# Kernel tuning notes

Measured on AMD Instinct MI355X. Metric: run time of the kernel, lower is better.

Reference implementation:

```python
import jax, jax.numpy as jnp
import numpy as np

D = 256; NH = 8; HD = D // NH; L = 4; P = 4; NQ = 900; BS = 8; DFFN = 1024
SHAPES = np.array([[128, 128], [64, 64], [32, 32], [16, 16]])  # (H, W) per level, static metadata
NV = int((SHAPES[:, 0] * SHAPES[:, 1]).sum())
EPS = 1e-6


def setup_inputs():
    key = jax.random.key(0)
    ks = iter(jax.random.split(key, 48))

    def nrm(shape, scale=0.02):
        return jax.random.normal(next(ks), shape, jnp.float32) * scale

    lsi = np.concatenate([[0], np.cumsum(SHAPES[:, 0] * SHAPES[:, 1])[:-1]]).astype(np.int64)
    return {
        'tgt': nrm((NQ, BS, D), 1.0),
        'tgt_query_pos': nrm((NQ, BS, D), 1.0),
        'tgt_reference_points': jax.random.uniform(next(ks), (NQ, BS, L, 2), jnp.float32),
        'memory': nrm((NV, BS, D), 1.0),
        'memory_spatial_shapes': jnp.asarray(SHAPES, jnp.int32),
        'memory_level_start_index': jnp.asarray(lsi, jnp.int32),
        'w_norm_sa': jnp.ones((D,), jnp.float32),
        'w_norm_ca': jnp.ones((D,), jnp.float32),
        'w_norm_ffn': jnp.ones((D,), jnp.float32),
        'ls_sa': jnp.full((D,), 1e-4, jnp.float32),
        'ls_ca': jnp.full((D,), 1e-4, jnp.float32),
        'ls_ffn': jnp.full((D,), 1e-4, jnp.float32),
        'Wq': nrm((D, D)), 'Wk': nrm((D, D)), 'Wv': nrm((D, D)),
        'bq': jnp.zeros((D,), jnp.float32), 'bk': jnp.zeros((D,), jnp.float32), 'bv': jnp.zeros((D,), jnp.float32),
        'Wo_sa': nrm((D, D)), 'bo_sa': jnp.zeros((D,), jnp.float32),
        'Wv_proj': nrm((D, D)), 'bv_proj': jnp.zeros((D,), jnp.float32),
        'W_off': nrm((NH * L * P * 2, D)), 'b_off': nrm((NH * L * P * 2,), 0.1),
        'W_attn': nrm((NH * L * P, D)), 'b_attn': jnp.zeros((NH * L * P,), jnp.float32),
        'W_out_ca': nrm((D, D)), 'bo_ca': jnp.zeros((D,), jnp.float32),
        'Wg': nrm((DFFN, D)), 'bg': jnp.zeros((DFFN,), jnp.float32),
        'Wu': nrm((DFFN, D)), 'bu': jnp.zeros((DFFN,), jnp.float32),
        'Wf': nrm((D, DFFN)), 'bf': jnp.zeros((D,), jnp.float32),
    }


def rmsnorm(x, w):
    return x * jax.lax.rsqrt(jnp.mean(x * x, axis=-1, keepdims=True) + EPS) * w


def ms_deform_sample(v, loc, attw):
    # v: (bs, nv, NH, HD); loc: (bs, nq, NH, L, P, 2) normalized (x, y); attw: (bs, nq, NH, L, P)
    bs, nq = loc.shape[0], loc.shape[1]
    out = jnp.zeros((bs, nq, NH, HD), loc.dtype)
    b_idx = jnp.arange(bs)[:, None, None, None]
    h_idx = jnp.arange(NH)[None, None, :, None]
    start = 0
    for l in range(L):
        Hl, Wl = int(SHAPES[l, 0]), int(SHAPES[l, 1])
        vf = v[:, start:start + Hl * Wl]  # (bs, Hl*Wl, NH, HD)
        start += Hl * Wl
        # grid_sample(align_corners=False, padding=zeros) pixel mapping
        x = loc[:, :, :, l, :, 0] * Wl - 0.5
        y = loc[:, :, :, l, :, 1] * Hl - 0.5
        x0 = jnp.floor(x)
        y0 = jnp.floor(y)
        acc = jnp.zeros((bs, nq, NH, P, HD), loc.dtype)
        for dx in (0, 1):
            for dy in (0, 1):
                xi = x0 + dx
                yi = y0 + dy
                w = (1.0 - jnp.abs(x - xi)) * (1.0 - jnp.abs(y - yi))
                valid = (xi >= 0) & (xi <= Wl - 1) & (yi >= 0) & (yi <= Hl - 1)
                w = jnp.where(valid, w, 0.0)
                idx = (jnp.clip(yi, 0, Hl - 1) * Wl + jnp.clip(xi, 0, Wl - 1)).astype(jnp.int32)
                acc = acc + w[..., None] * vf[b_idx, idx, h_idx]  # (bs, nq, NH, P, HD)
        out = out + jnp.einsum('bqhp,bqhpd->bqhd', attw[:, :, :, l], acc)
    return out


def reference(tgt, tgt_query_pos, tgt_reference_points, memory, memory_spatial_shapes,
              memory_level_start_index, w_norm_sa, w_norm_ca, w_norm_ffn, ls_sa, ls_ca, ls_ffn,
              Wq, Wk, Wv, bq, bk, bv, Wo_sa, bo_sa, Wv_proj, bv_proj, W_off, b_off, W_attn,
              b_attn, W_out_ca, bo_ca, Wg, bg, Wu, bu, Wf, bf):
    nq, bs, d = tgt.shape
    # --- self-attention (pre-norm + LayerScale residual) ---
    xn = rmsnorm(tgt, w_norm_sa)
    qk = xn + tgt_query_pos
    q = (qk @ Wq.T + bq).reshape(nq, bs, NH, HD)
    k = (qk @ Wk.T + bk).reshape(nq, bs, NH, HD)
    vv = (xn @ Wv.T + bv).reshape(nq, bs, NH, HD)
    scores = jnp.einsum('qbhd,kbhd->bhqk', q, k) * (1.0 / np.sqrt(HD))
    attn = jax.nn.softmax(scores, axis=-1)
    sa = jnp.einsum('bhqk,kbhd->qbhd', attn, vv).reshape(nq, bs, d) @ Wo_sa.T + bo_sa
    tgt = tgt + ls_sa * sa
    # --- multi-scale deformable cross-attention (identity=zeros in original) ---
    xn = rmsnorm(tgt, w_norm_ca)
    qca = jnp.swapaxes(xn + tgt_query_pos, 0, 1)  # (bs, nq, d)
    val = (jnp.swapaxes(memory, 0, 1) @ Wv_proj.T + bv_proj).reshape(bs, -1, NH, HD)
    off = (qca @ W_off.T + b_off).reshape(bs, nq, NH, L, P, 2)
    attw = jax.nn.softmax((qca @ W_attn.T + b_attn).reshape(bs, nq, NH, L * P), axis=-1)
    attw = attw.reshape(bs, nq, NH, L, P)
    norm = jnp.asarray(SHAPES[:, ::-1].copy(), jnp.float32)  # (W, H) per level
    ref = jnp.swapaxes(tgt_reference_points, 0, 1)  # (bs, nq, L, 2)
    loc = ref[:, :, None, :, None, :] + off / norm[None, None, None, :, None, :]
    ca = ms_deform_sample(val, loc, attw).reshape(bs, nq, d) @ W_out_ca.T + bo_ca
    tgt = tgt + ls_ca * jnp.swapaxes(ca, 0, 1)
    # --- SwiGLU FFN ---
    xn = rmsnorm(tgt, w_norm_ffn)
    ffn = (jax.nn.silu(xn @ Wg.T + bg) * (xn @ Wu.T + bu)) @ Wf.T + bf
    return tgt + ls_ffn * ffn
```

## Files before the change

kernel.cpp:

```cpp
#include <hip/hip_runtime.h>

typedef unsigned short ushort_t;
typedef unsigned int uint32;
typedef __bf16 bf16x8 __attribute__((ext_vector_type(8)));
typedef float f32x4 __attribute__((ext_vector_type(4)));
typedef ushort_t us4 __attribute__((ext_vector_type(4)));

#define D_    256
#define NH_   8
#define HD_   32
#define NQ_   900
#define BS_   8
#define TOK_  7200
#define NV_   21760
#define QP_   928
#define DFFN_ 1024

__device__ __forceinline__ ushort_t f2bf(float x) {
    union { float f; uint32 u; } v; v.f = x;
    uint32 r = v.u + 0x7FFFu + ((v.u >> 16) & 1u);
    return (ushort_t)(r >> 16);
}
__device__ __forceinline__ float bf2f(ushort_t h) {
    union { uint32 u; float f; } v; v.u = ((uint32)h) << 16;
    return v.f;
}
__device__ __forceinline__ int imin(int a, int b) { return a < b ? a : b; }
__device__ __forceinline__ int imax(int a, int b) { return a > b ? a : b; }

__global__ __launch_bounds__(256) void cvtall_k(
    const float* __restrict__ s0, const float* __restrict__ s1, const float* __restrict__ s2,
    const float* __restrict__ s3, const float* __restrict__ s4, const float* __restrict__ s5,
    const float* __restrict__ s6, const float* __restrict__ s7, const float* __restrict__ s8,
    const float* __restrict__ s9, const float* __restrict__ s10, ushort_t* __restrict__ dst,
    const float* __restrict__ bq, const float* __restrict__ bk, const float* __restrict__ bv,
    const float* __restrict__ boff, const float* __restrict__ battn,
    float* __restrict__ bias_qkv, float* __restrict__ bias_ol) {
    int tid = threadIdx.x;
    if (blockIdx.x == 0) {
        bias_qkv[tid] = bq[tid];
        bias_qkv[256 + tid] = bk[tid];
        bias_qkv[512 + tid] = bv[tid];
        bias_ol[tid] = boff[tid];
        if (tid < 128) bias_ol[256 + tid] = battn[tid];
    }
    int id = blockIdx.x * 256 + tid;
    const float* s; int off;
    if      (id <  16384) { s = s0;  off = id; }
    else if (id <  32768) { s = s1;  off = id - 16384; }
    else if (id <  49152) { s = s2;  off = id - 32768; }
    else if (id <  65536) { s = s3;  off = id - 49152; }
    else if (id <  81920) { s = s4;  off = id - 65536; }
    else if (id <  98304) { s = s5;  off = id - 81920; }
    else if (id < 114688) { s = s6;  off = id - 98304; }
    else if (id < 122880) { s = s7;  off = id - 114688; }
    else if (id < 188416) { s = s8;  off = id - 122880; }
    else if (id < 253952) { s = s9;  off = id - 188416; }
    else                  { s = s10; off = id - 253952; }
    f32x4 v = *(const f32x4*)(s + (size_t)off * 4);
    us4 t;
#pragma unroll
    for (int e = 0; e < 4; e++) t[e] = f2bf(v[e]);
    *(us4*)(dst + (size_t)id * 4) = t;
}

__global__ __launch_bounds__(256) void rms_k(const float* __restrict__ x,
                                             const float* __restrict__ pos,
                                             const float* __restrict__ wn,
                                             ushort_t* __restrict__ xn_out,
                                             ushort_t* __restrict__ qk_out) {
    const int r = blockIdx.x * 4 + (threadIdx.x >> 6);
    const int lane = threadIdx.x & 63;
    const size_t base = (size_t)r * D_ + lane * 4;
    f32x4 v = *(const f32x4*)(x + base);
    float ss = v[0] * v[0] + v[1] * v[1] + v[2] * v[2] + v[3] * v[3];
#pragma unroll
    for (int o = 32; o; o >>= 1) ss += __shfl_xor(ss, o, 64);
    float sc = rsqrtf(ss * (1.f / 256.f) + 1e-6f);
    f32x4 wv = *(const f32x4*)(wn + lane * 4);
    if (xn_out) {
        us4 t;
#pragma unroll
        for (int e = 0; e < 4; e++) t[e] = f2bf(v[e] * sc * wv[e]);
        *(us4*)(xn_out + base) = t;
    }
    if (qk_out) {
        f32x4 p = *(const f32x4*)(pos + base);
        us4 t;
#pragma unroll
        for (int e = 0; e < 4; e++) t[e] = f2bf(v[e] * sc * wv[e] + p[e]);
        *(us4*)(qk_out + base) = t;
    }
}

enum { EPI_RESID, EPI_QKV, EPI_OFFLOG };

template <int EPI, bool AF32, int BM, int BN, int WGM, int WGN, int TK>
__global__ __launch_bounds__(WGM * WGN * 64) void gemm2_k(
    const void* __restrict__ Ap, const void* __restrict__ Ap2,
    const ushort_t* __restrict__ Wp,
    const float* __restrict__ bias, void* __restrict__ outp, void* __restrict__ outp2,
    void* __restrict__ outp3, int M, int N, int swz,
    const float* __restrict__ resid, const float* __restrict__ ls, float scale) {
    constexpr int THREADS = WGM * WGN * 64;
    constexpr int NK  = TK / 32;
    constexpr int LDK = 40;
    constexpr int WR  = BM / WGM, WC = BN / WGN;
    constexpr int FM  = WR / 16,  FN = WC / 16;
    constexpr int ACH = AF32 ? (BM * 32 / 4 / THREADS) : (BM * 32 / 8 / THREADS);
    constexpr int BCH = BN * 32 / 8 / THREADS;

    __shared__ __align__(16) ushort_t As[2][BM * LDK];
    __shared__ __align__(16) ushort_t Bs[2][BN * LDK];

    const int tid = threadIdx.x, l = tid & 63, w = tid >> 6;
    const int wm = w % WGM, wn = w / WGM;
    int by = blockIdx.y;
    if (swz) { int cpx = gridDim.y >> 3; by = (by & 7) * cpx + (by >> 3); }
    const int m0 = by * BM, n0 = blockIdx.x * BN;
    const int lr = l & 15, lkb = (l >> 4) * 8;

    const void* Asel = (EPI == EPI_QKV && n0 >= 512) ? Ap2 : Ap;
    const ushort_t* Ab = (const ushort_t*)Asel;
    const float*    Af = (const float*)Asel;

    int aRow[ACH], aK[ACH], bRow[BCH], bK[BCH];
#pragma unroll
    for (int ch = 0; ch < ACH; ch++) {
        int cid = ch * THREADS + tid;
        if constexpr (AF32) { aRow[ch] = cid >> 3; aK[ch] = (cid & 7) * 4; }
        else                { aRow[ch] = cid >> 2; aK[ch] = (cid & 3) * 8; }
    }
#pragma unroll
    for (int ch = 0; ch < BCH; ch++) {
        int cid = ch * THREADS + tid;
        bRow[ch] = cid >> 2; bK[ch] = (cid & 3) * 8;
    }
    int aGRow[ACH];
#pragma unroll
    for (int ch = 0; ch < ACH; ch++) aGRow[ch] = imin(m0 + aRow[ch], M - 1);

    f32x4  aSTf[AF32 ? ACH : 1];
    bf16x8 aSTb[AF32 ? 1 : ACH];
    bf16x8 bST[BCH];

    auto load_regs = [&](int kt) {
        const int k0 = kt * 32;
#pragma unroll
        for (int ch = 0; ch < ACH; ch++) {
            if constexpr (AF32)
                aSTf[ch] = *(const f32x4*)(Af + (size_t)aGRow[ch] * TK + k0 + aK[ch]);
            else
                aSTb[ch] = *(const bf16x8*)(Ab + (size_t)aGRow[ch] * TK + k0 + aK[ch]);
        }
#pragma unroll
        for (int ch = 0; ch < BCH; ch++)
            bST[ch] = *(const bf16x8*)(Wp + (size_t)(n0 + bRow[ch]) * TK + k0 + bK[ch]);
    };
    auto write_lds = [&](int buf) {
#pragma unroll
        for (int ch = 0; ch < ACH; ch++) {
            if constexpr (AF32) {
                us4 t;
#pragma unroll
                for (int e = 0; e < 4; e++) t[e] = f2bf(aSTf[ch][e]);
                *(us4*)&As[buf][aRow[ch] * LDK + aK[ch]] = t;
            } else {
                *(bf16x8*)&As[buf][aRow[ch] * LDK + aK[ch]] = aSTb[ch];
            }
        }
#pragma unroll
        for (int ch = 0; ch < BCH; ch++)
            *(bf16x8*)&Bs[buf][bRow[ch] * LDK + bK[ch]] = bST[ch];
    };

    f32x4 acc[FM][FN];
#pragma unroll
    for (int i = 0; i < FM; i++)
#pragma unroll
        for (int j = 0; j < FN; j++) acc[i][j] = f32x4{0.f, 0.f, 0.f, 0.f};

    load_regs(0);
    write_lds(0);
    __syncthreads();

    for (int kt = 0; kt < NK; ++kt) {
        const int c = kt & 1;
        if (kt + 1 < NK) load_regs(kt + 1);

        bf16x8 af[FM], bf_[FN];
#pragma unroll
        for (int i = 0; i < FM; i++)
            af[i] = *(const bf16x8*)&As[c][(wm * WR + i * 16 + lr) * LDK + lkb];
#pragma unroll
        for (int j = 0; j < FN; j++)
            bf_[j] = *(const bf16x8*)&Bs[c][(wn * WC + j * 16 + lr) * LDK + lkb];
#pragma unroll
        for (int i = 0; i < FM; i++)
#pragma unroll
            for (int j = 0; j < FN; j++)
                acc[i][j] = __builtin_amdgcn_mfma_f32_16x16x32_bf16(af[i], bf_[j], acc[i][j], 0, 0, 0);

        if (kt + 1 < NK) write_lds(c ^ 1);
        __syncthreads();
    }

#pragma unroll
    for (int i = 0; i < FM; i++)
#pragma unroll
        for (int j = 0; j < FN; j++) {
            int col = n0 + wn * WC + j * 16 + lr;
            float bvv = bias[col];
#pragma unroll
            for (int e = 0; e < 4; e++) {
                int row = m0 + wm * WR + i * 16 + (l >> 4) * 4 + e;
                if (row >= M) continue;
                float v = acc[i][j][e] + bvv;
                if constexpr (EPI == EPI_RESID) {
                    size_t idx = (size_t)row * N + col;
                    ((float*)outp)[idx] = resid[idx] + ls[col] * v;
                } else if constexpr (EPI == EPI_QKV) {
                    int c2 = col & 255;
                    int q = row >> 3, bb = row & 7, h = c2 >> 5, hd = c2 & 31;
                    if (col < 256) {
                        ((ushort_t*)outp)[((bb * NH_ + h) * QP_ + q) * HD_ + hd] = f2bf(v * scale);
                    } else if (col < 512) {
                        ((ushort_t*)outp2)[((bb * NH_ + h) * QP_ + q) * HD_ + hd] = f2bf(v);
                    } else {
                        ((ushort_t*)outp3)[((bb * NH_ + h) * HD_ + hd) * QP_ + q] = f2bf(v);
                    }
                } else if constexpr (EPI == EPI_OFFLOG) {
                    if (col < 256) ((float*)outp)[(size_t)row * 256 + col] = v;
                    else           ((float*)outp2)[(size_t)row * 128 + col - 256] = v;
                }
            }
        }
}

__global__ __launch_bounds__(512) void gemm4_k(
    const float* __restrict__ Af, const ushort_t* __restrict__ Wp,
    const float* __restrict__ bias, ushort_t* __restrict__ outp, int swz) {
    constexpr int TK = 256, NK = 4, LDK = 72;
    __shared__ __align__(16) ushort_t As[2][64 * LDK];

    const int tid = threadIdx.x, l = tid & 63, w = tid >> 6;
    int by = blockIdx.y;
    if (swz) { int cpx = gridDim.y >> 3; by = (by & 7) * cpx + (by >> 3); }
    const int m0 = by * 64;
    const int lr = l & 15, g = l >> 4, lkb = g * 8;

    const int aRow = tid >> 3, aK = (tid & 7) * 4;
    const float* aPtr = Af + (size_t)(m0 + aRow) * TK + aK;
    f32x4 aST0, aST1;
    auto loadA = [&](int kt) {
        aST0 = *(const f32x4*)(aPtr + kt * 64);
        aST1 = *(const f32x4*)(aPtr + kt * 64 + 32);
    };
    auto writeA = [&](int buf) {
        us4 t0, t1;
#pragma unroll
        for (int e = 0; e < 4; e++) { t0[e] = f2bf(aST0[e]); t1[e] = f2bf(aST1[e]); }
        *(us4*)&As[buf][aRow * LDK + aK] = t0;
        *(us4*)&As[buf][aRow * LDK + 32 + aK] = t1;
    };

    const ushort_t* bPtr0 = Wp + (size_t)(w * 32 + lr) * TK + lkb;
    const ushort_t* bPtr1 = Wp + (size_t)(w * 32 + 16 + lr) * TK + lkb;

    f32x4 acc[4][2];
#pragma unroll
    for (int i = 0; i < 4; i++)
#pragma unroll
        for (int j = 0; j < 2; j++) acc[i][j] = f32x4{0.f, 0.f, 0.f, 0.f};

    bf16x8 bC[2][2], bN[2][2];
    loadA(0);
#pragma unroll
    for (int kk = 0; kk < 2; kk++) {
        bC[kk][0] = *(const bf16x8*)(bPtr0 + kk * 32);
        bC[kk][1] = *(const bf16x8*)(bPtr1 + kk * 32);
    }
    writeA(0);
    __syncthreads();

    for (int kt = 0; kt < NK; ++kt) {
        const int c = kt & 1;
        if (kt + 1 < NK) {
            loadA(kt + 1);
#pragma unroll
            for (int kk = 0; kk < 2; kk++) {
                bN[kk][0] = *(const bf16x8*)(bPtr0 + (kt + 1) * 64 + kk * 32);
                bN[kk][1] = *(const bf16x8*)(bPtr1 + (kt + 1) * 64 + kk * 32);
            }
        }
#pragma unroll
        for (int kk = 0; kk < 2; kk++) {
            bf16x8 af[4];
#pragma unroll
            for (int i = 0; i < 4; i++)
                af[i] = *(const bf16x8*)&As[c][(i * 16 + lr) * LDK + kk * 32 + lkb];
#pragma unroll
            for (int i = 0; i < 4; i++) {
                acc[i][0] = __builtin_amdgcn_mfma_f32_16x16x32_bf16(af[i], bC[kk][0], acc[i][0], 0, 0, 0);
                acc[i][1] = __builtin_amdgcn_mfma_f32_16x16x32_bf16(af[i], bC[kk][1], acc[i][1], 0, 0, 0);
            }
        }
        if (kt + 1 < NK) writeA(c ^ 1);
        __syncthreads();
#pragma unroll
        for (int kk = 0; kk < 2; kk++) {
            bC[kk][0] = bN[kk][0];
            bC[kk][1] = bN[kk][1];
        }
    }

#pragma unroll
    for (int i = 0; i < 4; i++)
#pragma unroll
        for (int j = 0; j < 2; j++) {
            int col = w * 32 + j * 16 + lr;
            float bvv = bias[col];
            int h = col >> 5, d = col & 31;
#pragma unroll
            for (int e = 0; e < 4; e++) {
                int row = m0 + i * 16 + g * 4 + e;
                int vv = row >> 3, bb = row & 7;
                outp[(((size_t)(bb * NH_ + h)) * NV_ + vv) * HD_ + d] = f2bf(acc[i][j][e] + bvv);
            }
        }
}

__global__ __launch_bounds__(256) void ffn2_k(
    const ushort_t* __restrict__ Ap, const ushort_t* __restrict__ Wg,
    const ushort_t* __restrict__ Wu, const float* __restrict__ bgp,
    const float* __restrict__ bup, ushort_t* __restrict__ outp, int M) {
    constexpr int TK = 256, NK = 4, LDK = 72;
    __shared__ __align__(16) ushort_t As[2][64 * LDK];

    const int tid = threadIdx.x, l = tid & 63, w = tid >> 6;
    const int m0 = blockIdx.y * 64, n0 = blockIdx.x * 128;
    const int lr = l & 15, g = l >> 4, lkb = g * 8;

    const int aRow = tid >> 2, aK = (tid & 3) * 16;
    const int aGRow = imin(m0 + aRow, M - 1);
    const ushort_t* aPtr = Ap + (size_t)aGRow * TK + aK;
    bf16x8 aST0, aST1;
    auto loadA = [&](int kt) {
        aST0 = *(const bf16x8*)(aPtr + kt * 64);
        aST1 = *(const bf16x8*)(aPtr + kt * 64 + 8);
    };
    auto writeA = [&](int buf) {
        *(bf16x8*)&As[buf][aRow * LDK + aK] = aST0;
        *(bf16x8*)&As[buf][aRow * LDK + aK + 8] = aST1;
    };

    const ushort_t* gP0 = Wg + (size_t)(n0 + w * 32 + lr) * TK + lkb;
    const ushort_t* gP1 = Wg + (size_t)(n0 + w * 32 + 16 + lr) * TK + lkb;
    const ushort_t* uP0 = Wu + (size_t)(n0 + w * 32 + lr) * TK + lkb;
    const ushort_t* uP1 = Wu + (size_t)(n0 + w * 32 + 16 + lr) * TK + lkb;

    f32x4 accG[4][2], accU[4][2];
#pragma unroll
    for (int i = 0; i < 4; i++)
#pragma unroll
        for (int j = 0; j < 2; j++) { accG[i][j] = f32x4{0,0,0,0}; accU[i][j] = f32x4{0,0,0,0}; }

    bf16x8 gC[2][2], uC[2][2], gN[2][2], uN[2][2];
    loadA(0);
#pragma unroll
    for (int kk = 0; kk < 2; kk++) {
        gC[kk][0] = *(const bf16x8*)(gP0 + kk * 32);
        gC[kk][1] = *(const bf16x8*)(gP1 + kk * 32);
        uC[kk][0] = *(const bf16x8*)(uP0 + kk * 32);
        uC[kk][1] = *(const bf16x8*)(uP1 + kk * 32);
    }
    writeA(0);
    __syncthreads();

    for (int kt = 0; kt < NK; ++kt) {
        const int c = kt & 1;
        if (kt + 1 < NK) {
            loadA(kt + 1);
#pragma unroll
            for (int kk = 0; kk < 2; kk++) {
                gN[kk][0] = *(const bf16x8*)(gP0 + (kt + 1) * 64 + kk * 32);
                gN[kk][1] = *(const bf16x8*)(gP1 + (kt + 1) * 64 + kk * 32);
                uN[kk][0] = *(const bf16x8*)(uP0 + (kt + 1) * 64 + kk * 32);
                uN[kk][1] = *(const bf16x8*)(uP1 + (kt + 1) * 64 + kk * 32);
            }
        }
#pragma unroll
        for (int kk = 0; kk < 2; kk++) {
            bf16x8 af[4];
#pragma unroll
            for (int i = 0; i < 4; i++)
                af[i] = *(const bf16x8*)&As[c][(i * 16 + lr) * LDK + kk * 32 + lkb];
#pragma unroll
            for (int i = 0; i < 4; i++) {
                accG[i][0] = __builtin_amdgcn_mfma_f32_16x16x32_bf16(af[i], gC[kk][0], accG[i][0], 0, 0, 0);
                accG[i][1] = __builtin_amdgcn_mfma_f32_16x16x32_bf16(af[i], gC[kk][1], accG[i][1], 0, 0, 0);
                accU[i][0] = __builtin_amdgcn_mfma_f32_16x16x32_bf16(af[i], uC[kk][0], accU[i][0], 0, 0, 0);
                accU[i][1] = __builtin_amdgcn_mfma_f32_16x16x32_bf16(af[i], uC[kk][1], accU[i][1], 0, 0, 0);
            }
        }
        if (kt + 1 < NK) writeA(c ^ 1);
        __syncthreads();
#pragma unroll
        for (int kk = 0; kk < 2; kk++) {
            gC[kk][0] = gN[kk][0]; gC[kk][1] = gN[kk][1];
            uC[kk][0] = uN[kk][0]; uC[kk][1] = uN[kk][1];
        }
    }

#pragma unroll
    for (int i = 0; i < 4; i++)
#pragma unroll
        for (int j = 0; j < 2; j++) {
            int col = n0 + w * 32 + j * 16 + lr;
            float bg_ = bgp[col], bu_ = bup[col];
#pragma unroll
            for (int e = 0; e < 4; e++) {
                int row = m0 + i * 16 + g * 4 + e;
                if (row >= M) continue;
                float gg = accG[i][j][e] + bg_;
                float uu = accU[i][j][e] + bu_;
                float s = gg / (1.f + __expf(-gg));
                outp[(size_t)row * DFFN_ + col] = f2bf(s * uu);
            }
        }
}

__global__ __launch_bounds__(256) void down_k(
    const ushort_t* __restrict__ Ap, const ushort_t* __restrict__ Wf,
    const float* __restrict__ bias, float* __restrict__ outp, int M,
    const float* __restrict__ resid, const float* __restrict__ ls) {
    constexpr int TK = 1024, NK = 16, LDK = 72;
    __shared__ __align__(16) ushort_t As[2][64 * LDK];

    const int tid = threadIdx.x, l = tid & 63, w = tid >> 6;
    const int m0 = blockIdx.y * 64, n0 = blockIdx.x * 128;
    const int lr = l & 15, g = l >> 4, lkb = g * 8;

    const int aRow = tid >> 2, aK = (tid & 3) * 16;
    const int aGRow = imin(m0 + aRow, M - 1);
    const ushort_t* aPtr = Ap + (size_t)aGRow * TK + aK;
    bf16x8 aST0, aST1;
    auto loadA = [&](int kt) {
        aST0 = *(const bf16x8*)(aPtr + kt * 64);
        aST1 = *(const bf16x8*)(aPtr + kt * 64 + 8);
    };
    auto writeA = [&](int buf) {
        *(bf16x8*)&As[buf][aRow * LDK + aK] = aST0;
        *(bf16x8*)&As[buf][aRow * LDK + aK + 8] = aST1;
    };

    const ushort_t* bP0 = Wf + (size_t)(n0 + w * 32 + lr) * TK + lkb;
    const ushort_t* bP1 = Wf + (size_t)(n0 + w * 32 + 16 + lr) * TK + lkb;

    f32x4 acc[4][2];
#pragma unroll
    for (int i = 0; i < 4; i++)
#pragma unroll
        for (int j = 0; j < 2; j++) acc[i][j] = f32x4{0.f, 0.f, 0.f, 0.f};

    bf16x8 bC[2][2], bN[2][2];
    loadA(0);
#pragma unroll
    for (int kk = 0; kk < 2; kk++) {
        bC[kk][0] = *(const bf16x8*)(bP0 + kk * 32);
        bC[kk][1] = *(const bf16x8*)(bP1 + kk * 32);
    }
    writeA(0);
    __syncthreads();

    for (int kt = 0; kt < NK; ++kt) {
        const int c = kt & 1;
        if (kt + 1 < NK) {
            loadA(kt + 1);
#pragma unroll
            for (int kk = 0; kk < 2; kk++) {
                bN[kk][0] = *(const bf16x8*)(bP0 + (kt + 1) * 64 + kk * 32);
                bN[kk][1] = *(const bf16x8*)(bP1 + (kt + 1) * 64 + kk * 32);
            }
        }
#pragma unroll
        for (int kk = 0; kk < 2; kk++) {
            bf16x8 af[4];
#pragma unroll
            for (int i = 0; i < 4; i++)
                af[i] = *(const bf16x8*)&As[c][(i * 16 + lr) * LDK + kk * 32 + lkb];
#pragma unroll
            for (int i = 0; i < 4; i++) {
                acc[i][0] = __builtin_amdgcn_mfma_f32_16x16x32_bf16(af[i], bC[kk][0], acc[i][0], 0, 0, 0);
                acc[i][1] = __builtin_amdgcn_mfma_f32_16x16x32_bf16(af[i], bC[kk][1], acc[i][1], 0, 0, 0);
            }
        }
        if (kt + 1 < NK) writeA(c ^ 1);
        __syncthreads();
#pragma unroll
        for (int kk = 0; kk < 2; kk++) {
            bC[kk][0] = bN[kk][0];
            bC[kk][1] = bN[kk][1];
        }
    }

#pragma unroll
    for (int i = 0; i < 4; i++)
#pragma unroll
        for (int j = 0; j < 2; j++) {
            int col = n0 + w * 32 + j * 16 + lr;
            float bvv = bias[col], lsc = ls[col];
#pragma unroll
            for (int e = 0; e < 4; e++) {
                int row = m0 + i * 16 + g * 4 + e;
                if (row >= M) continue;
                size_t idx = (size_t)row * 256 + col;
                outp[idx] = resid[idx] + lsc * (acc[i][j][e] + bvv);
            }
        }
}

__global__ __launch_bounds__(256) void attn2_k(const ushort_t* __restrict__ qb,
                                               const ushort_t* __restrict__ kb,
                                               const ushort_t* __restrict__ vtb,
                                               ushort_t* __restrict__ sab) {
    __shared__ __align__(16) ushort_t Pl[4][16 * 40];
    const int tid = threadIdx.x, l = tid & 63, w = tid >> 6;
    const int bh = blockIdx.y, b = bh >> 3, h = bh & 7;
    const int q0 = (blockIdx.x * 4 + w) * 16;
    if (q0 >= NQ_) return;
    const int q = l & 15, g = l >> 4;
    ushort_t* Pw = &Pl[w][0];

    const bf16x8 qf = *(const bf16x8*)(qb + ((size_t)bh * QP_ + q0 + q) * HD_ + g * 8);
    const ushort_t* kbase = kb + (size_t)bh * QP_ * HD_;
    const ushort_t* vbase = vtb + (size_t)bh * HD_ * QP_;

    f32x4 O0 = {0.f, 0.f, 0.f, 0.f}, O1 = {0.f, 0.f, 0.f, 0.f};
    float m = -1e30f, sl = 0.f;

    auto ldk = [&](int t, int u) {
        return *(const bf16x8*)(kbase + (size_t)(t * 32 + u * 16 + q) * HD_ + g * 8);
    };
    auto ldv = [&](int t, int dh) {
        return *(const bf16x8*)(vbase + (size_t)(dh * 16 + q) * QP_ + t * 32 + g * 8);
    };
    bf16x8 kA = ldk(0, 0), kB = ldk(0, 1), v0 = ldv(0, 0), v1 = ldv(0, 1);

    for (int t = 0; t < 29; ++t) {
        bf16x8 nkA, nkB, nv0, nv1;
        if (t < 28) { nkA = ldk(t + 1, 0); nkB = ldk(t + 1, 1); nv0 = ldv(t + 1, 0); nv1 = ldv(t + 1, 1); }
        const f32x4 z = {0.f, 0.f, 0.f, 0.f};
        f32x4 sA = __builtin_amdgcn_mfma_f32_16x16x32_bf16(kA, qf, z, 0, 0, 0);
        f32x4 sB = __builtin_amdgcn_mfma_f32_16x16x32_bf16(kB, qf, z, 0, 0, 0);
        if (t == 28) {
            int k0 = 896 + g * 4;
#pragma unroll
            for (int e = 0; e < 4; e++) {
                if (k0 + e >= NQ_)      sA[e] = -1e30f;
                if (k0 + 16 + e >= NQ_) sB[e] = -1e30f;
            }
        }
        float tm = fmaxf(fmaxf(fmaxf(sA[0], sA[1]), fmaxf(sA[2], sA[3])),
                         fmaxf(fmaxf(sB[0], sB[1]), fmaxf(sB[2], sB[3])));
        tm = fmaxf(tm, __shfl_xor(tm, 16, 64));
        tm = fmaxf(tm, __shfl_xor(tm, 32, 64));
        float mn = fmaxf(m, tm);
        float r = exp2f(m - mn);
        m = mn;
#pragma unroll
        for (int e = 0; e < 4; e++) { O0[e] *= r; O1[e] *= r; }
        float pA[4], pB[4], ps = 0.f;
#pragma unroll
        for (int e = 0; e < 4; e++) {
            pA[e] = exp2f(sA[e] - m); pB[e] = exp2f(sB[e] - m);
            ps += pA[e] + pB[e];
        }
        sl = sl * r + ps;
        uint32 a0, a1, b0, b1;
        asm("v_cvt_pk_bf16_f32 %0, %1, %2" : "=v"(a0) : "v"(pA[0]), "v"(pA[1]));
        asm("v_cvt_pk_bf16_f32 %0, %1, %2" : "=v"(a1) : "v"(pA[2]), "v"(pA[3]));
        asm("v_cvt_pk_bf16_f32 %0, %1, %2" : "=v"(b0) : "v"(pB[0]), "v"(pB[1]));
        asm("v_cvt_pk_bf16_f32 %0, %1, %2" : "=v"(b1) : "v"(pB[2]), "v"(pB[3]));
        { uint2 tt; tt.x = a0; tt.y = a1; *(uint2*)(Pw + q * 40 + g * 4) = tt; }
        { uint2 tt; tt.x = b0; tt.y = b1; *(uint2*)(Pw + q * 40 + 16 + g * 4) = tt; }
        bf16x8 pf = *(const bf16x8*)(Pw + q * 40 + g * 8);
        O0 = __builtin_amdgcn_mfma_f32_16x16x32_bf16(v0, pf, O0, 0, 0, 0);
        O1 = __builtin_amdgcn_mfma_f32_16x16x32_bf16(v1, pf, O1, 0, 0, 0);
        kA = nkA; kB = nkB; v0 = nv0; v1 = nv1;
    }

    sl += __shfl_xor(sl, 16, 64);
    sl += __shfl_xor(sl, 32, 64);
    float inv = 1.f / sl;
    int row_q = q0 + q;
    if (row_q < NQ_) {
        ushort_t* op = sab + ((size_t)row_q * BS_ + b) * D_ + h * HD_ + g * 4;
#pragma unroll
        for (int dh = 0; dh < 2; dh++) {
            f32x4 Ov = dh ? O1 : O0;
            float e0 = Ov[0] * inv, e1 = Ov[1] * inv, e2 = Ov[2] * inv, e3 = Ov[3] * inv;
            uint32 w0, w1;
            asm("v_cvt_pk_bf16_f32 %0, %1, %2" : "=v"(w0) : "v"(e0), "v"(e1));
            asm("v_cvt_pk_bf16_f32 %0, %1, %2" : "=v"(w1) : "v"(e2), "v"(e3));
            *(uint32*)(op + dh * 16) = w0;
            *(uint32*)(op + dh * 16 + 2) = w1;
        }
    }
}

__global__ __launch_bounds__(256) void deform_k(
    const float* __restrict__ offb, const float* __restrict__ logb,
    const float* __restrict__ refpts, const int* __restrict__ shapes,
    const int* __restrict__ lsi, const ushort_t* __restrict__ val,
    ushort_t* __restrict__ ca) {
    __shared__ float off_l[256];
    __shared__ float attw[128];
    const int r = blockIdx.x;
    const int b = r & 7;
    const int tid = threadIdx.x;

    off_l[tid] = offb[(size_t)r * 256 + tid];
    if (tid < 128) {
        float lg = logb[(size_t)r * 128 + tid];
        float m = lg;
#pragma unroll
        for (int o = 1; o < 16; o <<= 1) m = fmaxf(m, __shfl_xor(m, o, 16));
        float e = __expf(lg - m);
        float s = e;
#pragma unroll
        for (int o = 1; o < 16; o <<= 1) s += __shfl_xor(s, o, 16);
        attw[tid] = e / s;
    }
    __syncthreads();

    const int h = tid >> 5, d = tid & 31;
    const ushort_t* vb = val + ((size_t)(b * NH_ + h)) * NV_ * HD_;
    float acc = 0.f;
#pragma unroll
    for (int lvl = 0; lvl < 4; lvl++) {
        const int H = shapes[lvl * 2], W = shapes[lvl * 2 + 1];
        const int base = lsi[lvl];
        const float refx = refpts[(r * 4 + lvl) * 2];
        const float refy = refpts[(r * 4 + lvl) * 2 + 1];
#pragma unroll
        for (int p = 0; p < 4; p++) {
            int oi = ((h * 4 + lvl) * 4 + p) * 2;
            float x = (refx + off_l[oi] / (float)W) * (float)W - 0.5f;
            float y = (refy + off_l[oi + 1] / (float)H) * (float)H - 0.5f;
            float x0 = floorf(x), y0 = floorf(y);
            float fx = x - x0, fy = y - y0;
            int ix = (int)x0, iy = (int)y0;
            float sval = 0.f;
#pragma unroll
            for (int dy = 0; dy <= 1; dy++)
#pragma unroll
                for (int dx = 0; dx <= 1; dx++) {
                    int xi = ix + dx, yi = iy + dy;
                    float wq = (dx ? fx : 1.f - fx) * (dy ? fy : 1.f - fy);
                    if (xi < 0 || xi >= W || yi < 0 || yi >= H) wq = 0.f;
                    int cx = imin(imax(xi, 0), W - 1), cy = imin(imax(yi, 0), H - 1);
                    float vv = bf2f(vb[(size_t)(base + cy * W + cx) * HD_ + d]);
                    sval += wq * vv;
                }
            acc += attw[h * 16 + lvl * 4 + p] * sval;
        }
    }
    ca[(size_t)r * 256 + tid] = f2bf(acc);
}

extern "C" void kernel_launch(void* const* d_in, const int* in_sizes, int n_in,
                              void* d_out, int out_size, void* d_ws, size_t ws_size,
                              hipStream_t stream) {
    (void)in_sizes; (void)n_in; (void)out_size; (void)ws_size;
    const float* tgt    = (const float*)d_in[0];
    const float* qpos   = (const float*)d_in[1];
    const float* refp   = (const float*)d_in[2];
    const float* mem    = (const float*)d_in[3];
    const int*   shapes = (const int*)d_in[4];
    const int*   lsi    = (const int*)d_in[5];
    const float* wnsa   = (const float*)d_in[6];
    const float* wnca   = (const float*)d_in[7];
    const float* wnffn  = (const float*)d_in[8];
    const float* lssa   = (const float*)d_in[9];
    const float* lsca   = (const float*)d_in[10];
    const float* lsffn  = (const float*)d_in[11];
    const float* Wq = (const float*)d_in[12];
    const float* Wk = (const float*)d_in[13];
    const float* Wv = (const float*)d_in[14];
    const float* bq = (const float*)d_in[15];
    const float* bk = (const float*)d_in[16];
    const float* bvv = (const float*)d_in[17];
    const float* Wo_sa = (const float*)d_in[18];
    const float* bo_sa = (const float*)d_in[19];
    const float* Wv_proj = (const float*)d_in[20];
    const float* bv_proj = (const float*)d_in[21];
    const float* W_off = (const float*)d_in[22];
    const float* b_off = (const float*)d_in[23];
    const float* W_attn = (const float*)d_in[24];
    const float* b_attn = (const float*)d_in[25];
    const float* W_out = (const float*)d_in[26];
    const float* bo_ca = (const float*)d_in[27];
    const float* Wg = (const float*)d_in[28];
    const float* bg = (const float*)d_in[29];
    const float* Wu = (const float*)d_in[30];
    const float* bu = (const float*)d_in[31];
    const float* Wf = (const float*)d_in[32];
    const float* bff = (const float*)d_in[33];

    char* ws = (char*)d_ws;
    size_t o = 0;
    auto alloc = [&](size_t b) { size_t c = o; o += (b + 255) & ~(size_t)255; return c; };

    const size_t wq_o = alloc(65536 * 2), wk_o = alloc(65536 * 2), wv_o = alloc(65536 * 2);
    const size_t wosa_o = alloc(65536 * 2), wvp_o = alloc(65536 * 2), wout_o = alloc(65536 * 2);
    const size_t woff_o = alloc(65536 * 2), wattn_o = alloc(32768 * 2);
    const size_t wg_o = alloc(262144 * 2), wu_o = alloc(262144 * 2), wf_o = alloc(262144 * 2);
    const size_t bqkv_o = alloc(768 * 4), bol_o = alloc(384 * 4);
    const size_t xnsa_o = alloc((size_t)TOK_ * D_ * 2);
    const size_t qksa_o = alloc((size_t)TOK_ * D_ * 2);
    const size_t qkvBytes = (size_t)BS_ * NH_ * QP_ * HD_ * 2;
    const size_t qb_o = alloc(qkvBytes);
    const size_t kb_o = alloc(qkvBytes);
    const size_t vt_o = alloc(qkvBytes + 512);
    const size_t sa_o = alloc((size_t)TOK_ * D_ * 2);
    const size_t tgt1_o = alloc((size_t)TOK_ * D_ * 4);
    const size_t qca_o = alloc((size_t)TOK_ * D_ * 2);
    const size_t offb_o = alloc((size_t)TOK_ * 256 * 4);
    const size_t logit_o = alloc((size_t)TOK_ * 128 * 4);
    const size_t ca_o = alloc((size_t)TOK_ * D_ * 2);
    const size_t tgt2_o = alloc((size_t)TOK_ * D_ * 4);
    const size_t val_o = alloc((size_t)NV_ * BS_ * D_ * 2);
    const size_t h_o  = val_o;
    const size_t xn3_o = h_o + (size_t)TOK_ * DFFN_ * 2;

    dim3 blk(256);
    cvtall_k<<<dim3(319488 / 256), blk, 0, stream>>>(
        Wq, Wk, Wv, Wo_sa, Wv_proj, W_out, W_off, W_attn, Wg, Wu, Wf,
        (ushort_t*)(ws + wq_o),
        bq, bk, bvv, b_off, b_attn, (float*)(ws + bqkv_o), (float*)(ws + bol_o));


    rms_k<<<dim3(TOK_ / 4), blk, 0, stream>>>(tgt, qpos, wnsa,
                                              (ushort_t*)(ws + xnsa_o), (ushort_t*)(ws + qksa_o));
    const float QSC = 0.25503321550239915f;
    gemm2_k<EPI_QKV, false, 64, 128, 2, 2, 256><<<dim3(6, 113), blk, 0, stream>>>(
        ws + qksa_o, ws + xnsa_o, (ushort_t*)(ws + wq_o), (const float*)(ws + bqkv_o),
        ws + qb_o, ws + kb_o, ws + vt_o, TOK_, 768, 0, nullptr, nullptr, QSC);
    attn2_k<<<dim3(15, 64), blk, 0, stream>>>((ushort_t*)(ws + qb_o), (ushort_t*)(ws + kb_o),
                                              (ushort_t*)(ws + vt_o), (ushort_t*)(ws + sa_o));
    gemm2_k<EPI_RESID, false, 64, 128, 2, 2, 256><<<dim3(2, 113), blk, 0, stream>>>(
        ws + sa_o, nullptr, (ushort_t*)(ws + wosa_o), bo_sa, ws + tgt1_o, nullptr, nullptr,
        TOK_, 256, 0, tgt, lssa, 1.f);

    rms_k<<<dim3(TOK_ / 4), blk, 0, stream>>>((const float*)(ws + tgt1_o), qpos, wnca,
                                              nullptr, (ushort_t*)(ws + qca_o));
    gemm2_k<EPI_OFFLOG, false, 64, 128, 2, 2, 256><<<dim3(3, 113), blk, 0, stream>>>(
        ws + qca_o, nullptr, (ushort_t*)(ws + woff_o), (const float*)(ws + bol_o),
        ws + offb_o, ws + logit_o, nullptr, TOK_, 384, 0, nullptr, nullptr, 1.f);
    gemm4_k<<<dim3(1, 2720), dim3(512), 0, stream>>>(
        mem, (ushort_t*)(ws + wvp_o), bv_proj, (ushort_t*)(ws + val_o), 1);
    deform_k<<<dim3(TOK_), blk, 0, stream>>>(
        (const float*)(ws + offb_o), (const float*)(ws + logit_o), refp, shapes, lsi,
        (ushort_t*)(ws + val_o), (ushort_t*)(ws + ca_o));
    gemm2_k<EPI_RESID, false, 64, 128, 2, 2, 256><<<dim3(2, 113), blk, 0, stream>>>(
        ws + ca_o, nullptr, (ushort_t*)(ws + wout_o), bo_ca, ws + tgt2_o, nullptr, nullptr,
        TOK_, 256, 0, (const float*)(ws + tgt1_o), lsca, 1.f);

    rms_k<<<dim3(TOK_ / 4), blk, 0, stream>>>((const float*)(ws + tgt2_o), nullptr, wnffn,
                                              (ushort_t*)(ws + xn3_o), nullptr);
    ffn2_k<<<dim3(8, 113), blk, 0, stream>>>(
        (const ushort_t*)(ws + xn3_o), (const ushort_t*)(ws + wg_o),
        (const ushort_t*)(ws + wu_o), bg, bu, (ushort_t*)(ws + h_o), TOK_);
    down_k<<<dim3(2, 113), blk, 0, stream>>>(
        (const ushort_t*)(ws + h_o), (const ushort_t*)(ws + wf_o), bff,
        (float*)d_out, TOK_, (const float*)(ws + tgt2_o), lsffn);
}
```

Baseline: 322.9 us.

## Merge QKV projection and memory value projection into one launch

The self-attention QKV GEMM and the memory value-projection GEMM now run as one kernel with a combined grid. The first 678 blocks do the QKV tiles using only 256 of their 512 threads, and the remaining 2720 blocks do the value projection. The goal is to remove one launch and let the two independent GEMMs share the GPU at the same time. In exchange, half the threads idle in the QKV blocks, and the value projection now runs before attention instead of later. The generic gemm2 template drops its QKV and fp32-input variants.

```diff
diff --git a/kernel.cpp b/kernel.cpp
--- a/kernel.cpp
+++ b/kernel.cpp
@@ -93,21 +93,20 @@
     }
 }
 
-enum { EPI_RESID, EPI_QKV, EPI_OFFLOG };
-
-template <int EPI, bool AF32, int BM, int BN, int WGM, int WGN, int TK>
+enum { EPI_RESID, EPI_OFFLOG };
+
+template <int EPI, int BM, int BN, int WGM, int WGN, int TK>
 __global__ __launch_bounds__(WGM * WGN * 64) void gemm2_k(
-    const void* __restrict__ Ap, const void* __restrict__ Ap2,
-    const ushort_t* __restrict__ Wp,
+    const ushort_t* __restrict__ Ab, const ushort_t* __restrict__ Wp,
     const float* __restrict__ bias, void* __restrict__ outp, void* __restrict__ outp2,
-    void* __restrict__ outp3, int M, int N, int swz,
-    const float* __restrict__ resid, const float* __restrict__ ls, float scale) {
+    int M, int N,
+    const float* __restrict__ resid, const float* __restrict__ ls) {
     constexpr int THREADS = WGM * WGN * 64;
     constexpr int NK  = TK / 32;
     constexpr int LDK = 40;
     constexpr int WR  = BM / WGM, WC = BN / WGN;
     constexpr int FM  = WR / 16,  FN = WC / 16;
-    constexpr int ACH = AF32 ? (BM * 32 / 4 / THREADS) : (BM * 32 / 8 / THREADS);
+    constexpr int ACH = BM * 32 / 8 / THREADS;
     constexpr int BCH = BN * 32 / 8 / THREADS;
 
     __shared__ __align__(16) ushort_t As[2][BM * LDK];
@@ -115,21 +114,14 @@
 
     const int tid = threadIdx.x, l = tid & 63, w = tid >> 6;
     const int wm = w % WGM, wn = w / WGM;
-    int by = blockIdx.y;
-    if (swz) { int cpx = gridDim.y >> 3; by = (by & 7) * cpx + (by >> 3); }
-    const int m0 = by * BM, n0 = blockIdx.x * BN;
+    const int m0 = blockIdx.y * BM, n0 = blockIdx.x * BN;
     const int lr = l & 15, lkb = (l >> 4) * 8;
-
-    const void* Asel = (EPI == EPI_QKV && n0 >= 512) ? Ap2 : Ap;
-    const ushort_t* Ab = (const ushort_t*)Asel;
-    const float*    Af = (const float*)Asel;
 
     int aRow[ACH], aK[ACH], bRow[BCH], bK[BCH];
 #pragma unroll
     for (int ch = 0; ch < ACH; ch++) {
         int cid = ch * THREADS + tid;
-        if constexpr (AF32) { aRow[ch] = cid >> 3; aK[ch] = (cid & 7) * 4; }
-        else                { aRow[ch] = cid >> 2; aK[ch] = (cid & 3) * 8; }
+        aRow[ch] = cid >> 2; aK[ch] = (cid & 3) * 8;
     }
 #pragma unroll
     for (int ch = 0; ch < BCH; ch++) {
@@ -140,35 +132,22 @@
 #pragma unroll
     for (int ch = 0; ch < ACH; ch++) aGRow[ch] = imin(m0 + aRow[ch], M - 1);
 
-    f32x4  aSTf[AF32 ? ACH : 1];
-    bf16x8 aSTb[AF32 ? 1 : ACH];
+    bf16x8 aSTb[ACH];
     bf16x8 bST[BCH];
 
     auto load_regs = [&](int kt) {
         const int k0 = kt * 32;
 #pragma unroll
-        for (int ch = 0; ch < ACH; ch++) {
-            if constexpr (AF32)
-                aSTf[ch] = *(const f32x4*)(Af + (size_t)aGRow[ch] * TK + k0 + aK[ch]);
-            else
-                aSTb[ch] = *(const bf16x8*)(Ab + (size_t)aGRow[ch] * TK + k0 + aK[ch]);
-        }
+        for (int ch = 0; ch < ACH; ch++)
+            aSTb[ch] = *(const bf16x8*)(Ab + (size_t)aGRow[ch] * TK + k0 + aK[ch]);
 #pragma unroll
         for (int ch = 0; ch < BCH; ch++)
             bST[ch] = *(const bf16x8*)(Wp + (size_t)(n0 + bRow[ch]) * TK + k0 + bK[ch]);
     };
     auto write_lds = [&](int buf) {
 #pragma unroll
-        for (int ch = 0; ch < ACH; ch++) {
-            if constexpr (AF32) {
-                us4 t;
-#pragma unroll
-                for (int e = 0; e < 4; e++) t[e] = f2bf(aSTf[ch][e]);
-                *(us4*)&As[buf][aRow[ch] * LDK + aK[ch]] = t;
-            } else {
-                *(bf16x8*)&As[buf][aRow[ch] * LDK + aK[ch]] = aSTb[ch];
-            }
-        }
+        for (int ch = 0; ch < ACH; ch++)
+            *(bf16x8*)&As[buf][aRow[ch] * LDK + aK[ch]] = aSTb[ch];
 #pragma unroll
         for (int ch = 0; ch < BCH; ch++)
             *(bf16x8*)&Bs[buf][bRow[ch] * LDK + bK[ch]] = bST[ch];
@@ -219,17 +198,7 @@
                 if constexpr (EPI == EPI_RESID) {
                     size_t idx = (size_t)row * N + col;
                     ((float*)outp)[idx] = resid[idx] + ls[col] * v;
-                } else if constexpr (EPI == EPI_QKV) {
-                    int c2 = col & 255;
-                    int q = row >> 3, bb = row & 7, h = c2 >> 5, hd = c2 & 31;
-                    if (col < 256) {
-                        ((ushort_t*)outp)[((bb * NH_ + h) * QP_ + q) * HD_ + hd] = f2bf(v * scale);
-                    } else if (col < 512) {
-                        ((ushort_t*)outp2)[((bb * NH_ + h) * QP_ + q) * HD_ + hd] = f2bf(v);
-                    } else {
-                        ((ushort_t*)outp3)[((bb * NH_ + h) * HD_ + hd) * QP_ + q] = f2bf(v);
-                    }
-                } else if constexpr (EPI == EPI_OFFLOG) {
+                } else {
                     if (col < 256) ((float*)outp)[(size_t)row * 256 + col] = v;
                     else           ((float*)outp2)[(size_t)row * 128 + col - 256] = v;
                 }
@@ -237,97 +206,190 @@
         }
 }
 
-__global__ __launch_bounds__(512) void gemm4_k(
-    const float* __restrict__ Af, const ushort_t* __restrict__ Wp,
-    const float* __restrict__ bias, ushort_t* __restrict__ outp, int swz) {
-    constexpr int TK = 256, NK = 4, LDK = 72;
-    __shared__ __align__(16) ushort_t As[2][64 * LDK];
-
-    const int tid = threadIdx.x, l = tid & 63, w = tid >> 6;
-    int by = blockIdx.y;
-    if (swz) { int cpx = gridDim.y >> 3; by = (by & 7) * cpx + (by >> 3); }
-    const int m0 = by * 64;
+__global__ __launch_bounds__(512) void qkvval_k(
+    const ushort_t* __restrict__ qksa, const ushort_t* __restrict__ xnsa,
+    const ushort_t* __restrict__ wqkv, const float* __restrict__ bqkv,
+    ushort_t* __restrict__ qb, ushort_t* __restrict__ kb, ushort_t* __restrict__ vtb,
+    float qscale,
+    const float* __restrict__ mem, const ushort_t* __restrict__ wvp,
+    const float* __restrict__ bvp, ushort_t* __restrict__ valp) {
+    __shared__ __align__(16) char smem[30720];
+    const int rid = blockIdx.x;
+    const int tid = threadIdx.x, l = tid & 63;
     const int lr = l & 15, g = l >> 4, lkb = g * 8;
 
-    const int aRow = tid >> 3, aK = (tid & 7) * 4;
-    const float* aPtr = Af + (size_t)(m0 + aRow) * TK + aK;
-    f32x4 aST0, aST1;
-    auto loadA = [&](int kt) {
-        aST0 = *(const f32x4*)(aPtr + kt * 64);
-        aST1 = *(const f32x4*)(aPtr + kt * 64 + 32);
-    };
-    auto writeA = [&](int buf) {
-        us4 t0, t1;
-#pragma unroll
-        for (int e = 0; e < 4; e++) { t0[e] = f2bf(aST0[e]); t1[e] = f2bf(aST1[e]); }
-        *(us4*)&As[buf][aRow * LDK + aK] = t0;
-        *(us4*)&As[buf][aRow * LDK + 32 + aK] = t1;
-    };
-
-    const ushort_t* bPtr0 = Wp + (size_t)(w * 32 + lr) * TK + lkb;
-    const ushort_t* bPtr1 = Wp + (size_t)(w * 32 + 16 + lr) * TK + lkb;
-
-    f32x4 acc[4][2];
-#pragma unroll
-    for (int i = 0; i < 4; i++)
-#pragma unroll
-        for (int j = 0; j < 2; j++) acc[i][j] = f32x4{0.f, 0.f, 0.f, 0.f};
-
-    bf16x8 bC[2][2], bN[2][2];
-    loadA(0);
-#pragma unroll
-    for (int kk = 0; kk < 2; kk++) {
-        bC[kk][0] = *(const bf16x8*)(bPtr0 + kk * 32);
-        bC[kk][1] = *(const bf16x8*)(bPtr1 + kk * 32);
-    }
-    writeA(0);
-    __syncthreads();
-
-    for (int kt = 0; kt < NK; ++kt) {
-        const int c = kt & 1;
-        if (kt + 1 < NK) {
-            loadA(kt + 1);
+    if (rid < 678) {
+        ushort_t* As = (ushort_t*)smem;
+        ushort_t* Bs = (ushort_t*)(smem + 10240);
+        const bool act = tid < 256;
+        const int w4 = (tid >> 6) & 3, wm = w4 & 1, wn = w4 >> 1;
+        const int n0 = (rid % 6) * 128, m0 = (rid / 6) * 64;
+        const ushort_t* Ab = (n0 >= 512) ? xnsa : qksa;
+
+        const int t8 = tid & 255;
+        const int aRow = t8 >> 2, aK = (t8 & 3) * 8;
+        const int bRow0 = t8 >> 2, bK0 = (t8 & 3) * 8;
+        const int bRow1 = (256 + t8) >> 2, bK1 = ((256 + t8) & 3) * 8;
+        const int aGRow = imin(m0 + aRow, TOK_ - 1);
+
+        bf16x8 aST, bST0, bST1;
+        f32x4 acc[2][4];
+#pragma unroll
+        for (int i = 0; i < 2; i++)
+#pragma unroll
+            for (int j = 0; j < 4; j++) acc[i][j] = f32x4{0.f, 0.f, 0.f, 0.f};
+
+        auto load_regs = [&](int kt) {
+            const int k0 = kt * 32;
+            aST  = *(const bf16x8*)(Ab + (size_t)aGRow * 256 + k0 + aK);
+            bST0 = *(const bf16x8*)(wqkv + (size_t)(n0 + bRow0) * 256 + k0 + bK0);
+            bST1 = *(const bf16x8*)(wqkv + (size_t)(n0 + bRow1) * 256 + k0 + bK1);
+        };
+        auto write_lds = [&](int buf) {
+            *(bf16x8*)&As[buf * 2560 + aRow * 40 + aK] = aST;
+            *(bf16x8*)&Bs[buf * 5120 + bRow0 * 40 + bK0] = bST0;
+            *(bf16x8*)&Bs[buf * 5120 + bRow1 * 40 + bK1] = bST1;
+        };
+
+        if (act) { load_regs(0); write_lds(0); }
+        __syncthreads();
+
+        for (int kt = 0; kt < 8; ++kt) {
+            const int c = kt & 1;
+            if (act) {
+                if (kt + 1 < 8) load_regs(kt + 1);
+                bf16x8 af[2], bf_[4];
+#pragma unroll
+                for (int i = 0; i < 2; i++)
+                    af[i] = *(const bf16x8*)&As[c * 2560 + (wm * 32 + i * 16 + lr) * 40 + lkb];
+#pragma unroll
+                for (int j = 0; j < 4; j++)
+                    bf_[j] = *(const bf16x8*)&Bs[c * 5120 + (wn * 64 + j * 16 + lr) * 40 + lkb];
+#pragma unroll
+                for (int i = 0; i < 2; i++)
+#pragma unroll
+                    for (int j = 0; j < 4; j++)
+                        acc[i][j] = __builtin_amdgcn_mfma_f32_16x16x32_bf16(af[i], bf_[j], acc[i][j], 0, 0, 0);
+                if (kt + 1 < 8) write_lds(c ^ 1);
+            }
+            __syncthreads();
+        }
+
+        if (act) {
+#pragma unroll
+            for (int i = 0; i < 2; i++)
+#pragma unroll
+                for (int j = 0; j < 4; j++) {
+                    int col = n0 + wn * 64 + j * 16 + lr;
+                    float bvv = bqkv[col];
+#pragma unroll
+                    for (int e = 0; e < 4; e++) {
+                        int row = m0 + wm * 32 + i * 16 + g * 4 + e;
+                        if (row >= TOK_) continue;
+                        float v = acc[i][j][e] + bvv;
+                        int c2 = col & 255;
+                        int q = row >> 3, bb = row & 7, h = c2 >> 5, hd = c2 & 31;
+                        if (col < 256)
+                            qb[((bb * NH_ + h) * QP_ + q) * HD_ + hd] = f2bf(v * qscale);
+                        else if (col < 512)
+                            kb[((bb * NH_ + h) * QP_ + q) * HD_ + hd] = f2bf(v);
+                        else
+                            vtb[((bb * NH_ + h) * HD_ + hd) * QP_ + q] = f2bf(v);
+                    }
+                }
+        }
+        return;
+    }
+
+    {
+        constexpr int TK = 256, NK = 4, LDK = 72;
+        ushort_t* As = (ushort_t*)smem;
+
+        const int vid = rid - 678;
+        const int by = (vid & 7) * 340 + (vid >> 3);
+        const int w = tid >> 6;
+        const int m0 = by * 64;
+
+        const int aRow = tid >> 3, aK = (tid & 7) * 4;
+        const float* aPtr = mem + (size_t)(m0 + aRow) * TK + aK;
+        f32x4 aST0, aST1;
+        auto loadA = [&](int kt) {
+            aST0 = *(const f32x4*)(aPtr + kt * 64);
+            aST1 = *(const f32x4*)(aPtr + kt * 64 + 32);
+        };
+        auto writeA = [&](int buf) {
+            us4 t0, t1;
+#pragma unroll
+            for (int e = 0; e < 4; e++) { t0[e] = f2bf(aST0[e]); t1[e] = f2bf(aST1[e]); }
+            *(us4*)&As[buf * 4608 + aRow * LDK + aK] = t0;
+            *(us4*)&As[buf * 4608 + aRow * LDK + 32 + aK] = t1;
+        };
+
+        const ushort_t* bPtr0 = wvp + (size_t)(w * 32 + lr) * TK + lkb;
+        const ushort_t* bPtr1 = wvp + (size_t)(w * 32 + 16 + lr) * TK + lkb;
+
+        f32x4 acc[4][2];
+#pragma unroll
+        for (int i = 0; i < 4; i++)
+#pragma unroll
+            for (int j = 0; j < 2; j++) acc[i][j] = f32x4{0.f, 0.f, 0.f, 0.f};
+
+        bf16x8 bC[2][2], bN[2][2];
+        loadA(0);
+#pragma unroll
+        for (int kk = 0; kk < 2; kk++) {
+            bC[kk][0] = *(const bf16x8*)(bPtr0 + kk * 32);
+            bC[kk][1] = *(const bf16x8*)(bPtr1 + kk * 32);
+        }
+        writeA(0);
+        __syncthreads();
+
+        for (int kt = 0; kt < NK; ++kt) {
+            const int c = kt & 1;
+            if (kt + 1 < NK) {
+                loadA(kt + 1);
+#pragma unroll
+                for (int kk = 0; kk < 2; kk++) {
+                    bN[kk][0] = *(const bf16x8*)(bPtr0 + (kt + 1) * 64 + kk * 32);
+                    bN[kk][1] = *(const bf16x8*)(bPtr1 + (kt + 1) * 64 + kk * 32);
+                }
+            }
 #pragma unroll
             for (int kk = 0; kk < 2; kk++) {
-                bN[kk][0] = *(const bf16x8*)(bPtr0 + (kt + 1) * 64 + kk * 32);
-                bN[kk][1] = *(const bf16x8*)(bPtr1 + (kt + 1) * 64 + kk * 32);
-            }
-        }
-#pragma unroll
-        for (int kk = 0; kk < 2; kk++) {
-            bf16x8 af[4];
-#pragma unroll
-            for (int i = 0; i < 4; i++)
-                af[i] = *(const bf16x8*)&As[c][(i * 16 + lr) * LDK + kk * 32 + lkb];
-#pragma unroll
-            for (int i = 0; i < 4; i++) {
-                acc[i][0] = __builtin_amdgcn_mfma_f32_16x16x32_bf16(af[i], bC[kk][0], acc[i][0], 0, 0, 0);
-                acc[i][1] = __builtin_amdgcn_mfma_f32_16x16x32_bf16(af[i], bC[kk][1], acc[i][1], 0, 0, 0);
-            }
-        }
-        if (kt + 1 < NK) writeA(c ^ 1);
-        __syncthreads();
-#pragma unroll
-        for (int kk = 0; kk < 2; kk++) {
-            bC[kk][0] = bN[kk][0];
-            bC[kk][1] = bN[kk][1];
-        }
-    }
-
-#pragma unroll
-    for (int i = 0; i < 4; i++)
-#pragma unroll
-        for (int j = 0; j < 2; j++) {
-            int col = w * 32 + j * 16 + lr;
-            float bvv = bias[col];
-            int h = col >> 5, d = col & 31;
-#pragma unroll
-            for (int e = 0; e < 4; e++) {
-                int row = m0 + i * 16 + g * 4 + e;
-                int vv = row >> 3, bb = row & 7;
-                outp[(((size_t)(bb * NH_ + h)) * NV_ + vv) * HD_ + d] = f2bf(acc[i][j][e] + bvv);
-            }
-        }
+                bf16x8 af[4];
+#pragma unroll
+                for (int i = 0; i < 4; i++)
+                    af[i] = *(const bf16x8*)&As[c * 4608 + (i * 16 + lr) * LDK + kk * 32 + lkb];
+#pragma unroll
+                for (int i = 0; i < 4; i++) {
+                    acc[i][0] = __builtin_amdgcn_mfma_f32_16x16x32_bf16(af[i], bC[kk][0], acc[i][0], 0, 0, 0);
+                    acc[i][1] = __builtin_amdgcn_mfma_f32_16x16x32_bf16(af[i], bC[kk][1], acc[i][1], 0, 0, 0);
+                }
+            }
+            if (kt + 1 < NK) writeA(c ^ 1);
+            __syncthreads();
+#pragma unroll
+            for (int kk = 0; kk < 2; kk++) {
+                bC[kk][0] = bN[kk][0];
+                bC[kk][1] = bN[kk][1];
+            }
+        }
+
+#pragma unroll
+        for (int i = 0; i < 4; i++)
+#pragma unroll
+            for (int j = 0; j < 2; j++) {
+                int col = w * 32 + j * 16 + lr;
+                float bvv = bvp[col];
+                int h = col >> 5, d = col & 31;
+#pragma unroll
+                for (int e = 0; e < 4; e++) {
+                    int row = m0 + i * 16 + g * 4 + e;
+                    int vv = row >> 3, bb = row & 7;
+                    valp[(((size_t)(bb * NH_ + h)) * NV_ + vv) * HD_ + d] = f2bf(acc[i][j][e] + bvv);
+                }
+            }
+    }
 }
 
 __global__ __launch_bounds__(256) void ffn2_k(
@@ -744,28 +806,28 @@
     rms_k<<<dim3(TOK_ / 4), blk, 0, stream>>>(tgt, qpos, wnsa,
                                               (ushort_t*)(ws + xnsa_o), (ushort_t*)(ws + qksa_o));
     const float QSC = 0.25503321550239915f;
-    gemm2_k<EPI_QKV, false, 64, 128, 2, 2, 256><<<dim3(6, 113), blk, 0, stream>>>(
-        ws + qksa_o, ws + xnsa_o, (ushort_t*)(ws + wq_o), (const float*)(ws + bqkv_o),
-        ws + qb_o, ws + kb_o, ws + vt_o, TOK_, 768, 0, nullptr, nullptr, QSC);
+    qkvval_k<<<dim3(678 + 2720), dim3(512), 0, stream>>>(
+        (const ushort_t*)(ws + qksa_o), (const ushort_t*)(ws + xnsa_o),
+        (const ushort_t*)(ws + wq_o), (const float*)(ws + bqkv_o),
+        (ushort_t*)(ws + qb_o), (ushort_t*)(ws + kb_o), (ushort_t*)(ws + vt_o), QSC,
+        mem, (const ushort_t*)(ws + wvp_o), bv_proj, (ushort_t*)(ws + val_o));
     attn2_k<<<dim3(15, 64), blk, 0, stream>>>((ushort_t*)(ws + qb_o), (ushort_t*)(ws + kb_o),
                                               (ushort_t*)(ws + vt_o), (ushort_t*)(ws + sa_o));
-    gemm2_k<EPI_RESID, false, 64, 128, 2, 2, 256><<<dim3(2, 113), blk, 0, stream>>>(
-        ws + sa_o, nullptr, (ushort_t*)(ws + wosa_o), bo_sa, ws + tgt1_o, nullptr, nullptr,
-        TOK_, 256, 0, tgt, lssa, 1.f);
+    gemm2_k<EPI_RESID, 64, 128, 2, 2, 256><<<dim3(2, 113), blk, 0, stream>>>(
+        (const ushort_t*)(ws + sa_o), (ushort_t*)(ws + wosa_o), bo_sa, ws + tgt1_o, nullptr,
+        TOK_, 256, tgt, lssa);
 
     rms_k<<<dim3(TOK_ / 4), blk, 0, stream>>>((const float*)(ws + tgt1_o), qpos, wnca,
                                               nullptr, (ushort_t*)(ws + qca_o));
-    gemm2_k<EPI_OFFLOG, false, 64, 128, 2, 2, 256><<<dim3(3, 113), blk, 0, stream>>>(
-        ws + qca_o, nullptr, (ushort_t*)(ws + woff_o), (const float*)(ws + bol_o),
-        ws + offb_o, ws + logit_o, nullptr, TOK_, 384, 0, nullptr, nullptr, 1.f);
-    gemm4_k<<<dim3(1, 2720), dim3(512), 0, stream>>>(
-        mem, (ushort_t*)(ws + wvp_o), bv_proj, (ushort_t*)(ws + val_o), 1);
+    gemm2_k<EPI_OFFLOG, 64, 128, 2, 2, 256><<<dim3(3, 113), blk, 0, stream>>>(
+        (const ushort_t*)(ws + qca_o), (ushort_t*)(ws + woff_o), (const float*)(ws + bol_o),
+        ws + offb_o, ws + logit_o, TOK_, 384, nullptr, nullptr);
     deform_k<<<dim3(TOK_), blk, 0, stream>>>(
         (const float*)(ws + offb_o), (const float*)(ws + logit_o), refp, shapes, lsi,
         (ushort_t*)(ws + val_o), (ushort_t*)(ws + ca_o));
-    gemm2_k<EPI_RESID, false, 64, 128, 2, 2, 256><<<dim3(2, 113), blk, 0, stream>>>(
-        ws + ca_o, nullptr, (ushort_t*)(ws + wout_o), bo_ca, ws + tgt2_o, nullptr, nullptr,
-        TOK_, 256, 0, (const float*)(ws + tgt1_o), lsca, 1.f);
+    gemm2_k<EPI_RESID, 64, 128, 2, 2, 256><<<dim3(2, 113), blk, 0, stream>>>(
+        (const ushort_t*)(ws + ca_o), (ushort_t*)(ws + wout_o), bo_ca, ws + tgt2_o, nullptr,
+        TOK_, 256, (const float*)(ws + tgt1_o), lsca);
 
     rms_k<<<dim3(TOK_ / 4), blk, 0, stream>>>((const float*)(ws + tgt2_o), nullptr, wnffn,
                                               (ushort_t*)(ws + xn3_o), nullptr);
```

Measured after the change: 317.4 us (median of 2 runs). About the same (-1.7%).
